# Optimization experiments

Hardware: AMD Instinct MI355X
Metric: run time of the kernel (lower is better)

## Reference

```python
import jax, jax.numpy as jnp
import numpy as np

B, C, E, H = 8, 2048, 1024, 128


def setup_inputs() -> dict:
    key = jax.random.key(0)
    kx, kq, kk, kv = jax.random.split(key, 4)
    scale = 1.0 / np.sqrt(E)
    return {
        "x": jax.random.normal(kx, (B, C, E), dtype=jnp.float32),
        "Wq": jax.random.normal(kq, (E, H), dtype=jnp.float32) * scale,
        "Wk": jax.random.normal(kk, (E, H), dtype=jnp.float32) * scale,
        "Wv": jax.random.normal(kv, (E, H), dtype=jnp.float32) * scale,
    }


def reference(x, Wq, Wk, Wv):
    # x: (B, C, E); projections -> (B, C, H)
    q = jnp.einsum("bce,eh->bch", x, Wq)
    k = jnp.einsum("bce,eh->bch", x, Wk)
    v = jnp.einsum("bce,eh->bch", x, Wv)
    # NOTE: original scales by sqrt(embed_size), not head_size
    scores = jnp.einsum("bqh,bkh->bqk", q, k) / jnp.sqrt(jnp.asarray(E, x.dtype))
    Cq = x.shape[1]
    causal = jnp.tril(jnp.ones((Cq, Cq), dtype=bool))
    scores = jnp.where(causal, scores, -jnp.inf)
    weights = jax.nn.softmax(scores, axis=-1)  # (B, C, C)
    out = jnp.einsum("bqk,bkh->bqh", weights, v)
    return out
```

## Files before the change

kernel.cpp:

```cpp
#include <hip/hip_runtime.h>
#include <hip/hip_bf16.h>

#define BATCH 8
#define CTX   2048
#define EMB   1024
#define HD    128
#define VSTR  2080

using bf16x8 = __attribute__((ext_vector_type(8))) short;
using fx4    = __attribute__((ext_vector_type(4))) float;

__device__ __forceinline__ ushort f2bf(float f) {
    union { float f; unsigned u; } v; v.f = f;
    unsigned u = v.u;
    u += 0x7fffu + ((u >> 16) & 1u);
    return (ushort)(u >> 16);
}

__device__ __forceinline__ unsigned cvtpk(float a, float b) {
    unsigned r;
    asm("v_cvt_pk_bf16_f32 %0, %1, %2" : "=v"(r) : "v"(a), "v"(b));
    return r;
}

__device__ __forceinline__ float exp2a(float x) {
    float r;
    asm("v_exp_f32 %0, %1" : "=v"(r) : "v"(x));
    return r;
}

__device__ __forceinline__ void gload16(const void* g, void* l) {
    __builtin_amdgcn_global_load_lds(
        (const __attribute__((address_space(1))) unsigned*)g,
        (__attribute__((address_space(3))) unsigned*)l, 16, 0, 0);
}

__global__ __launch_bounds__(256) void wt_kernel(
        const float* __restrict__ Wq, const float* __restrict__ Wk,
        const float* __restrict__ Wv, ushort* __restrict__ Wt) {
    __shared__ ushort lds[64][65];
    const int w  = blockIdx.z;
    const int e0 = blockIdx.x * 64;
    const int h0 = blockIdx.y * 64;
    const float* W = (w == 0) ? Wq : (w == 1) ? Wk : Wv;
    const int tl = threadIdx.x & 63;
    const int tg = threadIdx.x >> 6;
#pragma unroll
    for (int rr = 0; rr < 16; ++rr) {
        const int el = rr * 4 + tg;
        lds[el][tl] = f2bf(W[(size_t)(e0 + el) * HD + h0 + tl]);
    }
    __syncthreads();
#pragma unroll
    for (int rr = 0; rr < 16; ++rr) {
        const int hl = rr * 4 + tg;
        Wt[((size_t)w * HD + h0 + hl) * EMB + e0 + tl] = lds[tl][hl];
    }
}

__global__ __launch_bounds__(256) void proj_kernel(
        const float* __restrict__ x, const ushort* __restrict__ Wt,
        ushort* __restrict__ q, ushort* __restrict__ k, ushort* __restrict__ vt) {
    __shared__ __align__(16) float  As[32 * 64];
    __shared__ __align__(16) ushort Bs[192 * 64];

    const int t    = threadIdx.x;
    const int wave = t >> 6;
    const int lane = t & 63;
    const int lo = lane & 15, hi = lane >> 4;
    const int brow = blockIdx.x * 32;
    const int bcol = blockIdx.y * 192;
    const int kph  = (blockIdx.x ^ (blockIdx.y << 3)) & 15;

    const char* Ab = (const char*)As;
    const char* Bb = (const char*)Bs;

    fx4 acc[2][3];
#pragma unroll
    for (int m2 = 0; m2 < 2; m2++)
#pragma unroll
        for (int n = 0; n < 3; n++) acc[m2][n] = fx4{0.f, 0.f, 0.f, 0.f};

    const int arow_s = t >> 4;
    const int acol_s = ((t & 15) ^ (arow_s & 7)) << 2;
    const int brow_s = t >> 3;
    const int bcol_s = ((t & 7) ^ (brow_s & 7)) << 3;
    const int ldsbase = wave * 1024;

    for (int i = 0; i < 16; ++i) {
        const int k0 = ((i + kph) & 15) << 6;
#pragma unroll
        for (int r = 0; r < 2; r++)
            gload16(x + (size_t)(brow + r * 16 + arow_s) * EMB + k0 + acol_s,
                    (char*)As + r * 4096 + ldsbase);
#pragma unroll
        for (int r = 0; r < 6; r++)
            gload16(Wt + (size_t)(bcol + r * 32 + brow_s) * EMB + k0 + bcol_s,
                    (char*)Bs + r * 4096 + ldsbase);
        __syncthreads();

#pragma unroll
        for (int ks = 0; ks < 2; ks++) {
            bf16x8 af[2], bfr[3];
#pragma unroll
            for (int m2 = 0; m2 < 2; m2++) {
                const int rowA = m2 * 16 + lo;
                const unsigned sw = (rowA & 7) << 4;
                const unsigned ub = rowA * 256 + ks * 128 + hi * 32;
                fx4 a0 = *(const fx4*)(Ab + (ub ^ sw));
                fx4 a1 = *(const fx4*)(Ab + ((ub + 16) ^ sw));
                union { unsigned u[4]; bf16x8 v; } pk;
                pk.u[0] = cvtpk(a0[0], a0[1]);
                pk.u[1] = cvtpk(a0[2], a0[3]);
                pk.u[2] = cvtpk(a1[0], a1[1]);
                pk.u[3] = cvtpk(a1[2], a1[3]);
                af[m2] = pk.v;
            }
#pragma unroll
            for (int n = 0; n < 3; n++) {
                const int rowB = wave * 48 + n * 16 + lo;
                const unsigned ub = rowB * 128 + ks * 64 + hi * 16;
                bfr[n] = *(const bf16x8*)(Bb + (ub ^ ((rowB & 7) << 4)));
            }
#pragma unroll
            for (int m2 = 0; m2 < 2; m2++)
#pragma unroll
                for (int n = 0; n < 3; n++)
                    acc[m2][n] = __builtin_amdgcn_mfma_f32_16x16x32_bf16(af[m2], bfr[n], acc[m2][n], 0, 0, 0);
        }
        __syncthreads();
    }

    const float qscale = 0.045084219f;
#pragma unroll
    for (int n = 0; n < 3; n++) {
        const int col = bcol + wave * 48 + n * 16 + lo;
        const int bnn = col >> 7;
        const int cc  = col & 127;
#pragma unroll
        for (int m2 = 0; m2 < 2; m2++) {
#pragma unroll
            for (int j = 0; j < 4; j++) {
                const int r = brow + m2 * 16 + hi * 4 + j;
                if (bnn == 0)      q[(size_t)r * HD + cc] = f2bf(acc[m2][n][j] * qscale);
                else if (bnn == 1) k[(size_t)r * HD + cc] = f2bf(acc[m2][n][j]);
                else {
                    const int bb2 = r >> 11, ccc = r & (CTX - 1);
                    vt[((size_t)bb2 * HD + cc) * VSTR + ccc] = f2bf(acc[m2][n][j]);
                }
            }
        }
    }
}

__global__ __launch_bounds__(256) void attn_kernel(
        const ushort* __restrict__ q, const ushort* __restrict__ k,
        const ushort* __restrict__ vt, float* __restrict__ out) {
    __shared__ __align__(16) char Ks[2][4][8192];
    __shared__ __align__(16) char p_lds[4][1280];

    const int id   = blockIdx.x;
    const int b    = id & 7;
    const int p    = id >> 3;
    const int t    = threadIdx.x;
    const int w    = t >> 6;
    const int lane = t & 63;
    const int lo = lane & 15, hi = lane >> 4;

    const ushort* qb = q  + (size_t)b * CTX * HD;
    const ushort* kb = k  + (size_t)b * CTX * HD;
    const ushort* vb = vt + (size_t)b * HD * VSTR;

    float* oB  = (float*)&Ks[0][0][0];
    float* mlB = (float*)&Ks[0][3][0];

#define KSTAGE(bi, kv0_) do {                                                  \
    _Pragma("unroll")                                                          \
    for (int r = 0; r < 8; ++r) {                                              \
        const int rl  = r * 4 + (lane >> 4);                                   \
        const int key = (rl >> 1) & 7;                                         \
        gload16(kb + (size_t)((kv0_) + w * 32 + rl) * HD + (((lane & 15) ^ key) << 3), \
                Ks[bi][w] + r * 1024);                                         \
    }                                                                          \
} while (0)

    for (int phase = 0; phase < 2; ++phase) {
        const int qt = phase ? p : (127 - p);
        const int q0 = qt * 16;
        const int nkv = qt / 8 + 1;

        bf16x8 qf[4];
#pragma unroll
        for (int ks = 0; ks < 4; ks++)
            qf[ks] = *(const bf16x8*)(qb + (size_t)(q0 + lo) * HD + ks * 32 + hi * 8);

        fx4 o[8];
#pragma unroll
        for (int h = 0; h < 8; h++) o[h] = fx4{0.f, 0.f, 0.f, 0.f};
        float m[4], l[4];
#pragma unroll
        for (int j = 0; j < 4; j++) { m[j] = 0.f; l[j] = 0.f; }

        KSTAGE(0, 0);

        for (int it = 0; it < nkv; ++it) {
            const int kv0 = it * 128;
            bf16x8 vf[8];
#pragma unroll
            for (int h = 0; h < 8; h++)
                vf[h] = *(const bf16x8*)(vb + (size_t)(h * 16 + lo) * VSTR + kv0 + w * 32 + hi * 8);
            __builtin_amdgcn_sched_barrier(0);
            if (it + 1 < nkv) {
                KSTAGE((it + 1) & 1, kv0 + 128);
                __builtin_amdgcn_sched_barrier(0);
                asm volatile("s_waitcnt vmcnt(16)" ::: "memory");
            } else {
                asm volatile("s_waitcnt vmcnt(8)" ::: "memory");
            }
            __builtin_amdgcn_sched_barrier(0);

            const char* Kb = Ks[it & 1][w];
            fx4 s[2];
            s[0] = fx4{0.f, 0.f, 0.f, 0.f};
            s[1] = fx4{0.f, 0.f, 0.f, 0.f};
            __builtin_amdgcn_s_setprio(1);
#pragma unroll
            for (int n2 = 0; n2 < 2; n2++) {
                const int rl = 2 * lo + n2;
#pragma unroll
                for (int ks = 0; ks < 4; ks++) {
                    bf16x8 kf = *(const bf16x8*)(Kb + rl * 256 + ((ks * 64 + hi * 16) ^ ((lo & 7) << 4)));
                    s[n2] = __builtin_amdgcn_mfma_f32_16x16x32_bf16(qf[ks], kf, s[n2], 0, 0, 0);
                }
            }
            __builtin_amdgcn_s_setprio(0);

            const bool diag = (kv0 + 128 > q0);
            float pmax[4];
            int allok = 1;
#pragma unroll
            for (int j = 0; j < 4; j++) {
                const int r = q0 + hi * 4 + j;
                if (diag) {
                    const int c0 = kv0 + w * 32 + 2 * lo;
                    if (c0 > r)     s[0][j] = -INFINITY;
                    if (c0 + 1 > r) s[1][j] = -INFINITY;
                }
                pmax[j] = fmaxf(s[0][j], s[1][j]);
                allok &= (pmax[j] <= m[j] + 23.0f);
            }
            if (!__all(allok)) {
#pragma unroll
                for (int j = 0; j < 4; j++) {
                    float mx = pmax[j];
                    mx = fmaxf(mx, __shfl_xor(mx, 1));
                    mx = fmaxf(mx, __shfl_xor(mx, 2));
                    mx = fmaxf(mx, __shfl_xor(mx, 4));
                    mx = fmaxf(mx, __shfl_xor(mx, 8));
                    const float mn = fmaxf(m[j], mx);
                    const float f  = exp2a(m[j] - mn);
                    l[j] *= f;
#pragma unroll
                    for (int h = 0; h < 8; h++) o[h][j] *= f;
                    m[j] = mn;
                }
            }
#pragma unroll
            for (int j = 0; j < 4; j++) {
                const float p0 = exp2a(s[0][j] - m[j]);
                const float p1 = exp2a(s[1][j] - m[j]);
                l[j] += p0 + p1;
                *(unsigned*)(p_lds[w] + (hi * 4 + j) * 80 + lo * 4) = cvtpk(p0, p1);
            }
            asm volatile("" ::: "memory");
            bf16x8 pa = *(const bf16x8*)(p_lds[w] + lo * 80 + hi * 16);
            __builtin_amdgcn_s_setprio(1);
#pragma unroll
            for (int h = 0; h < 8; h++)
                o[h] = __builtin_amdgcn_mfma_f32_16x16x32_bf16(pa, vf[h], o[h], 0, 0, 0);
            __builtin_amdgcn_s_setprio(0);
        }

#pragma unroll
        for (int j = 0; j < 4; j++) {
            l[j] += __shfl_xor(l[j], 1);
            l[j] += __shfl_xor(l[j], 2);
            l[j] += __shfl_xor(l[j], 4);
            l[j] += __shfl_xor(l[j], 8);
        }

        __syncthreads();
        if (w > 0) {
#pragma unroll
            for (int j = 0; j < 4; j++) {
                const int row = hi * 4 + j;
                if (lo == 0) { mlB[(w - 1) * 32 + row] = m[j]; mlB[(w - 1) * 32 + 16 + row] = l[j]; }
#pragma unroll
                for (int h = 0; h < 8; h++)
                    oB[(w - 1) * 2048 + row * 128 + h * 16 + lo] = o[h][j];
            }
        }
        __syncthreads();
        if (w == 0) {
            float* ob = out + ((size_t)b * CTX + q0) * HD;
#pragma unroll
            for (int j = 0; j < 4; j++) {
                const int row = hi * 4 + j;
                float mp[3], lp[3];
                float mt = m[j];
#pragma unroll
                for (int pp = 0; pp < 3; pp++) {
                    mp[pp] = mlB[pp * 32 + row];
                    lp[pp] = mlB[pp * 32 + 16 + row];
                    mt = fmaxf(mt, mp[pp]);
                }
                const float f0 = exp2a(m[j] - mt);
                float fp[3];
#pragma unroll
                for (int pp = 0; pp < 3; pp++) fp[pp] = exp2a(mp[pp] - mt);
                const float inv = 1.0f / (l[j] * f0 + lp[0] * fp[0] + lp[1] * fp[1] + lp[2] * fp[2]);
#pragma unroll
                for (int h = 0; h < 8; h++) {
                    float acc = o[h][j] * f0;
#pragma unroll
                    for (int pp = 0; pp < 3; pp++)
                        acc += oB[pp * 2048 + row * 128 + h * 16 + lo] * fp[pp];
                    ob[row * HD + h * 16 + lo] = acc * inv;
                }
            }
        }
        __syncthreads();
        asm volatile("s_waitcnt vmcnt(0)" ::: "memory");
    }
#undef KSTAGE
}

extern "C" void kernel_launch(void* const* d_in, const int* in_sizes, int n_in,
                              void* d_out, int out_size, void* d_ws, size_t ws_size,
                              hipStream_t stream) {
    const float* x  = (const float*)d_in[0];
    const float* Wq = (const float*)d_in[1];
    const float* Wk = (const float*)d_in[2];
    const float* Wv = (const float*)d_in[3];

    ushort* Wt = (ushort*)d_ws;
    ushort* qw = (ushort*)((char*)d_ws + 786432);
    ushort* kw = qw + (size_t)BATCH * CTX * HD;
    ushort* vw = kw + (size_t)BATCH * CTX * HD;

    wt_kernel<<<dim3(EMB / 64, HD / 64, 3), 256, 0, stream>>>(Wq, Wk, Wv, Wt);
    proj_kernel<<<dim3(512, 2), 256, 0, stream>>>(x, Wt, qw, kw, vw);
    attn_kernel<<<512, 256, 0, stream>>>(qw, kw, vw, (float*)d_out);
}
```

Measured before the change: 84.79 us.

## Software-pipeline projection GEMM with double-buffered A and per-wave private B tiles

```diff
diff --git a/kernel.cpp b/kernel.cpp
--- a/kernel.cpp
+++ b/kernel.cpp
@@ -61,7 +61,7 @@
 __global__ __launch_bounds__(256) void proj_kernel(
         const float* __restrict__ x, const ushort* __restrict__ Wt,
         ushort* __restrict__ q, ushort* __restrict__ k, ushort* __restrict__ vt) {
-    __shared__ __align__(16) float  As[32 * 64];
+    __shared__ __align__(16) float  As[2][32 * 64];
     __shared__ __align__(16) ushort Bs[192 * 64];
 
     const int t    = threadIdx.x;
@@ -72,9 +72,6 @@
     const int bcol = blockIdx.y * 192;
     const int kph  = (blockIdx.x ^ (blockIdx.y << 3)) & 15;
 
-    const char* Ab = (const char*)As;
-    const char* Bb = (const char*)Bs;
-
     fx4 acc[2][3];
 #pragma unroll
     for (int m2 = 0; m2 < 2; m2++)
@@ -83,30 +80,49 @@
 
     const int arow_s = t >> 4;
     const int acol_s = ((t & 15) ^ (arow_s & 7)) << 2;
-    const int brow_s = t >> 3;
-    const int bcol_s = ((t & 7) ^ (brow_s & 7)) << 3;
-    const int ldsbase = wave * 1024;
+    const char* Bw = (const char*)Bs + wave * 6144;
+
+#define ASTAGE(bi, k0_) do {                                                    \
+    _Pragma("unroll")                                                           \
+    for (int r = 0; r < 2; ++r)                                                 \
+        gload16(x + (size_t)(brow + r * 16 + arow_s) * EMB + (k0_) + acol_s,    \
+                (char*)As[bi] + r * 4096 + wave * 1024);                        \
+} while (0)
+
+#define BSTAGE(k0_) do {                                                        \
+    _Pragma("unroll")                                                           \
+    for (int r = 0; r < 6; ++r) {                                               \
+        const int ci  = r * 64 + lane;                                          \
+        const int rowL = ci >> 3;                                               \
+        const int slot = (ci & 7) ^ (rowL & 7);                                 \
+        gload16(Wt + (size_t)(bcol + wave * 48 + rowL) * EMB + (k0_) + (slot << 3), \
+                (char*)Bs + wave * 6144 + r * 1024);                            \
+    }                                                                           \
+} while (0)
+
+    {
+        const int k0 = (kph & 15) << 6;
+        ASTAGE(0, k0);
+        BSTAGE(k0);
+    }
 
     for (int i = 0; i < 16; ++i) {
-        const int k0 = ((i + kph) & 15) << 6;
-#pragma unroll
-        for (int r = 0; r < 2; r++)
-            gload16(x + (size_t)(brow + r * 16 + arow_s) * EMB + k0 + acol_s,
-                    (char*)As + r * 4096 + ldsbase);
-#pragma unroll
-        for (int r = 0; r < 6; r++)
-            gload16(Wt + (size_t)(bcol + r * 32 + brow_s) * EMB + k0 + bcol_s,
-                    (char*)Bs + r * 4096 + ldsbase);
-        __syncthreads();
-
-#pragma unroll
-        for (int ks = 0; ks < 2; ks++) {
-            bf16x8 af[2], bfr[3];
-#pragma unroll
-            for (int m2 = 0; m2 < 2; m2++) {
-                const int rowA = m2 * 16 + lo;
-                const unsigned sw = (rowA & 7) << 4;
-                const unsigned ub = rowA * 256 + ks * 128 + hi * 32;
+        asm volatile("s_waitcnt vmcnt(0)" ::: "memory");
+        __builtin_amdgcn_sched_barrier(0);
+        __builtin_amdgcn_s_barrier();
+        __builtin_amdgcn_sched_barrier(0);
+
+        if (i + 1 < 16) ASTAGE((i + 1) & 1, (((i + 1 + kph) & 15) << 6));
+
+        const char* Ab = (const char*)As[i & 1];
+        bf16x8 afr[2][2];
+#pragma unroll
+        for (int m2 = 0; m2 < 2; m2++) {
+            const int rowA = m2 * 16 + lo;
+            const unsigned sw = (rowA & 7) << 4;
+#pragma unroll
+            for (int ks2 = 0; ks2 < 2; ks2++) {
+                const unsigned ub = rowA * 256 + ks2 * 128 + hi * 32;
                 fx4 a0 = *(const fx4*)(Ab + (ub ^ sw));
                 fx4 a1 = *(const fx4*)(Ab + ((ub + 16) ^ sw));
                 union { unsigned u[4]; bf16x8 v; } pk;
@@ -114,22 +130,36 @@
                 pk.u[1] = cvtpk(a0[2], a0[3]);
                 pk.u[2] = cvtpk(a1[0], a1[1]);
                 pk.u[3] = cvtpk(a1[2], a1[3]);
-                af[m2] = pk.v;
-            }
+                afr[m2][ks2] = pk.v;
+            }
+        }
+        bf16x8 bfr[2][3];
+#pragma unroll
+        for (int ks2 = 0; ks2 < 2; ks2++)
 #pragma unroll
             for (int n = 0; n < 3; n++) {
-                const int rowB = wave * 48 + n * 16 + lo;
-                const unsigned ub = rowB * 128 + ks * 64 + hi * 16;
-                bfr[n] = *(const bf16x8*)(Bb + (ub ^ ((rowB & 7) << 4)));
-            }
+                const int rowL = n * 16 + lo;
+                const unsigned ub = rowL * 128 + ks2 * 64 + hi * 16;
+                bfr[ks2][n] = *(const bf16x8*)(Bw + (ub ^ ((lo & 7) << 4)));
+            }
+        asm volatile("s_waitcnt lgkmcnt(0)" ::: "memory");
+        __builtin_amdgcn_sched_barrier(0);
+        if (i + 1 < 16) BSTAGE((((i + 1 + kph) & 15) << 6));
+        __builtin_amdgcn_sched_barrier(0);
+
+        __builtin_amdgcn_s_setprio(1);
+#pragma unroll
+        for (int ks2 = 0; ks2 < 2; ks2++)
 #pragma unroll
             for (int m2 = 0; m2 < 2; m2++)
 #pragma unroll
                 for (int n = 0; n < 3; n++)
-                    acc[m2][n] = __builtin_amdgcn_mfma_f32_16x16x32_bf16(af[m2], bfr[n], acc[m2][n], 0, 0, 0);
-        }
-        __syncthreads();
-    }
+                    acc[m2][n] = __builtin_amdgcn_mfma_f32_16x16x32_bf16(
+                        afr[m2][ks2], bfr[ks2][n], acc[m2][n], 0, 0, 0);
+        __builtin_amdgcn_s_setprio(0);
+    }
+#undef ASTAGE
+#undef BSTAGE
 
     const float qscale = 0.045084219f;
 #pragma unroll
```

After: 82.34 us. 1.03x faster.
